# Kernel optimization log

Hardware: AMD Instinct MI355X
Metric: run time of the kernel (lower is better)

Reference implementation:

```python
import jax, jax.numpy as jnp
import numpy as np

N, C, T, V = 64, 64, 256, 25
REL, OUT = 8, 64
ALPHA = 1.0


def setup_inputs() -> dict:
    key = jax.random.key(0)
    ks = jax.random.split(key, 10)
    s = lambda k, shape: jax.random.normal(k, shape, dtype=jnp.float32) * 0.05
    return {
        "x": jax.random.normal(ks[0], (N, C, T, V), dtype=jnp.float32),
        "A": jax.random.normal(ks[1], (V, V), dtype=jnp.float32),
        "w1": s(ks[2], (REL, C)), "b1": s(ks[3], (REL,)),
        "w2": s(ks[4], (REL, C)), "b2": s(ks[5], (REL,)),
        "w3": s(ks[6], (OUT, C)), "b3": s(ks[7], (OUT,)),
        "w4": s(ks[8], (OUT, REL)), "b4": s(ks[9], (OUT,)),
    }


def reference(x, A, w1, b1, w2, b2, w3, b3, w4, b4):
    # 1x1 conv commutes with the temporal mean, so reduce T first (same math).
    xm = jnp.mean(x, axis=2)                                   # [N, C, V]
    x1 = jnp.einsum('ncv,rc->nrv', xm, w1) + b1[:, None]        # [N, R, V]
    x2 = jnp.einsum('ncv,rc->nrv', xm, w2) + b2[:, None]        # [N, R, V]
    x3 = jnp.einsum('nctv,oc->notv', x, w3) + b3[:, None, None] # [N, O, T, V]
    # dynamic topology: tanh of broadcast difference -> [N, R, V, V]
    adj = jnp.tanh(x1[:, :, :, None] - x2[:, :, None, :])
    # conv4 (1x1 over VxV) then scale + static adjacency
    d = jnp.einsum('nruv,or->nouv', adj, w4) + b4[:, None, None]
    d = d * ALPHA + A[None, None]                               # [N, O, V, V]
    # graph aggregation: out[n,o,t,v] = sum_u d[n,o,u,v] * x3[n,o,t,u]
    return jnp.einsum('nouv,notu->notv', d, x3)
```

## Files before the change

kernel.cpp:

```cpp
#include <hip/hip_runtime.h>

#define N_ 64
#define C_ 64
#define T_ 256
#define V_ 25
#define R_ 8
#define O_ 64
constexpr int TV = T_ * V_;
constexpr float INV_T = 1.0f / (float)T_;
constexpr int TC = 16;
constexpr int NPOS = TC * V_;
constexpr int NT = NPOS / 16;
constexpr int DP = 32;
constexpr int UPAD = 40;
constexpr int X3S = 16 * UPAD + 8;

typedef __attribute__((ext_vector_type(8))) short s8v;
typedef __attribute__((ext_vector_type(4))) short s4v;
typedef __attribute__((ext_vector_type(4))) float f4v;

__device__ __forceinline__ unsigned short f2bf(float f) {
    union { float f; unsigned u; } v; v.f = f;
    unsigned r = v.u + 0x7FFFu + ((v.u >> 16) & 1u);
    return (unsigned short)(r >> 16);
}

__global__ __launch_bounds__(256) void k_mean(const float* __restrict__ x,
                                              float* __restrict__ xm) {
    __shared__ float part[8 * V_];
    const int bid = blockIdx.x;
    const int tid = threadIdx.x;
    const float* xp = x + (size_t)bid * TV;
    if (tid < 200) {
        const int vid = tid % V_;
        const int seg = tid / V_;
        float s = 0.f;
        const float* p = xp + seg * 32 * V_ + vid;
        #pragma unroll
        for (int j = 0; j < 32; ++j) s += p[j * V_];
        part[tid] = s;
    }
    __syncthreads();
    if (tid < V_) {
        float s = 0.f;
        #pragma unroll
        for (int k = 0; k < 8; ++k) s += part[k * V_ + tid];
        xm[(size_t)bid * V_ + tid] = s * INV_T;
    }
}

__global__ __launch_bounds__(256) void k_dmat(const float* __restrict__ xm,
                                              const float* __restrict__ A,
                                              const float* __restrict__ w1,
                                              const float* __restrict__ b1,
                                              const float* __restrict__ w2,
                                              const float* __restrict__ b2,
                                              const float* __restrict__ w4,
                                              const float* __restrict__ b4,
                                              unsigned short* __restrict__ dT) {
    __shared__ float xms[C_][V_];
    __shared__ float x1s[R_][V_];
    __shared__ float x2s[R_][V_];
    const int n  = blockIdx.x;
    const int og = blockIdx.y * 8;
    const int tid = threadIdx.x;

    for (int i = tid; i < C_ * V_; i += 256)
        xms[i / V_][i % V_] = xm[(size_t)n * C_ * V_ + i];
    __syncthreads();

    for (int i = tid; i < 2 * R_ * V_; i += 256) {
        const int j = i % (R_ * V_);
        const int r = j / V_, v = j % V_;
        const bool first = (i < R_ * V_);
        const float* w = first ? w1 : w2;
        float acc = first ? b1[r] : b2[r];
        #pragma unroll
        for (int c = 0; c < C_; ++c) acc += w[r * C_ + c] * xms[c][v];
        if (first) x1s[r][v] = acc;
        else       x2s[r][v] = acc;
    }
    __syncthreads();

    unsigned short* dn = dT + (size_t)n * O_ * DP * DP;
    for (int p = tid; p < DP * DP; p += 256) {
        const int v = p >> 5, u = p & 31;
        if (u < V_ && v < V_) {
            float adjr[R_];
            #pragma unroll
            for (int r = 0; r < R_; ++r) adjr[r] = tanhf(x1s[r][u] - x2s[r][v]);
            const float a = A[u * V_ + v];
            #pragma unroll
            for (int oo = 0; oo < 8; ++oo) {
                const int o = og + oo;
                float acc = b4[o];
                #pragma unroll
                for (int r = 0; r < R_; ++r) acc = fmaf(w4[o * R_ + r], adjr[r], acc);
                dn[(size_t)o * DP * DP + p] = f2bf(acc + a);
            }
        } else {
            #pragma unroll
            for (int oo = 0; oo < 8; ++oo)
                dn[(size_t)(og + oo) * DP * DP + p] = 0;
        }
    }
}

__global__ __launch_bounds__(512) void k_F(const float* __restrict__ x,
                                           const float* __restrict__ w3,
                                           const float* __restrict__ b3,
                                           const unsigned short* __restrict__ dT,
                                           float* __restrict__ out) {
    __shared__ __align__(16) unsigned short x3b[16 * X3S];

    const int n    = blockIdx.y;
    const int tc   = blockIdx.x;
    const int tid  = threadIdx.x;
    const int lane = tid & 63;
    const int wave = tid >> 6;
    const int l16  = lane & 15;
    const int lg   = lane >> 4;

    if (tid < 256) {
        const int o_l = tid >> 4, t = tid & 15;
        *(s8v*)&x3b[o_l * X3S + t * UPAD + 24] = (s8v)0;
    }
    __syncthreads();

    const float* xbase = x + (size_t)n * C_ * TV + tc * NPOS;
    s8v bfr[4][2];
    #pragma unroll
    for (int i = 0; i < 4; ++i) {
        const int nt = wave + 8 * i;
        if (nt < NT) {
            const int pos = nt * 16 + l16;
            #pragma unroll
            for (int kh = 0; kh < 2; ++kh) {
                s8v f;
                #pragma unroll
                for (int j = 0; j < 8; ++j)
                    f[j] = (short)f2bf(xbase[(size_t)(kh * 32 + lg * 8 + j) * TV + pos]);
                bfr[i][kh] = f;
            }
        }
    }

    const unsigned short* dn = dT + (size_t)n * O_ * DP * DP;
    float* on = out + (size_t)n * O_ * TV + tc * NPOS;

    #pragma unroll 1
    for (int h = 0; h < 4; ++h) {
        s8v afr[2];
        #pragma unroll
        for (int kh = 0; kh < 2; ++kh) {
            const float* wp = w3 + (h * 16 + l16) * C_ + kh * 32 + lg * 8;
            s8v f;
            #pragma unroll
            for (int j = 0; j < 8; ++j) f[j] = (short)f2bf(wp[j]);
            afr[kh] = f;
        }
        const f4v b3h = *(const f4v*)(b3 + h * 16 + lg * 4);

        #pragma unroll
        for (int i = 0; i < 4; ++i) {
            const int nt = wave + 8 * i;
            if (nt < NT) {
                const int pos = nt * 16 + l16;
                const int t = pos / 25, u = pos - 25 * t;
                f4v acc = (f4v)0.f;
                acc = __builtin_amdgcn_mfma_f32_16x16x32_bf16(afr[0], bfr[i][0], acc, 0, 0, 0);
                acc = __builtin_amdgcn_mfma_f32_16x16x32_bf16(afr[1], bfr[i][1], acc, 0, 0, 0);
                #pragma unroll
                for (int r = 0; r < 4; ++r)
                    x3b[(lg * 4 + r) * X3S + t * UPAD + u] = f2bf(acc[r] + b3h[r]);
            }
        }
        __syncthreads();

        #pragma unroll
        for (int oo = 0; oo < 2; ++oo) {
            const int o_l = wave * 2 + oo;
            const int o_g = h * 16 + o_l;
            const unsigned short* dp = dn + (size_t)o_g * DP * DP;
            const s8v bv0 = *(const s8v*)(dp + l16 * DP + lg * 8);
            const s8v bv1 = *(const s8v*)(dp + (16 + l16) * DP + lg * 8);
            const s8v av  = *(const s8v*)&x3b[o_l * X3S + l16 * UPAD + lg * 8];
            f4v c0 = (f4v)0.f, c1 = (f4v)0.f;
            c0 = __builtin_amdgcn_mfma_f32_16x16x32_bf16(av, bv0, c0, 0, 0, 0);
            c1 = __builtin_amdgcn_mfma_f32_16x16x32_bf16(av, bv1, c1, 0, 0, 0);
            float* ob = on + (size_t)o_g * TV;
            #pragma unroll
            for (int r = 0; r < 4; ++r) {
                const int t = lg * 4 + r;
                ob[t * 25 + l16] = c0[r];
                if (l16 < 9) ob[t * 25 + 16 + l16] = c1[r];
            }
        }
        __syncthreads();
    }
}

extern "C" void kernel_launch(void* const* d_in, const int* in_sizes, int n_in,
                              void* d_out, int out_size, void* d_ws, size_t ws_size,
                              hipStream_t stream) {
    const float* x  = (const float*)d_in[0];
    const float* A  = (const float*)d_in[1];
    const float* w1 = (const float*)d_in[2];
    const float* b1 = (const float*)d_in[3];
    const float* w2 = (const float*)d_in[4];
    const float* b2 = (const float*)d_in[5];
    const float* w3 = (const float*)d_in[6];
    const float* b3 = (const float*)d_in[7];
    const float* w4 = (const float*)d_in[8];
    const float* b4 = (const float*)d_in[9];

    float* out = (float*)d_out;
    float* xm  = (float*)d_ws;
    unsigned short* dTm = (unsigned short*)(xm + (size_t)N_ * C_ * V_);

    k_mean<<<N_ * C_, 256, 0, stream>>>(x, xm);
    k_dmat<<<dim3(N_, 8), 256, 0, stream>>>(xm, A, w1, b1, w2, b2, w4, b4, dTm);
    k_F<<<dim3(T_ / TC, N_), 512, 0, stream>>>(x, w3, b3, dTm, out);
}
```

Baseline: 86.82 us.

## Fuse temporal mean with bf16 transpose of x staged in output buffer

Replaces the per-channel mean kernel with a tiled prep kernel that loads x once through shared memory. It accumulates the temporal mean with atomics and writes a bf16 K-contiguous transposed copy of x into the output buffer as scratch. k_F then reads that packed copy with vector loads instead of strided scalar fp32 loads plus per-element conversion. This adds a memset, atomics and an extra write/read pass through the output buffer. Correctness depends on each k_F block consuming its own scratch region before overwriting it.

```diff
diff --git a/kernel.cpp b/kernel.cpp
--- a/kernel.cpp
+++ b/kernel.cpp
@@ -14,10 +14,12 @@
 constexpr int DP = 32;
 constexpr int UPAD = 40;
 constexpr int X3S = 16 * UPAD + 8;
+constexpr int CH = 32;
+constexpr int LROW = 402;
 
 typedef __attribute__((ext_vector_type(8))) short s8v;
-typedef __attribute__((ext_vector_type(4))) short s4v;
 typedef __attribute__((ext_vector_type(4))) float f4v;
+typedef __attribute__((ext_vector_type(2))) float f2v;
 
 __device__ __forceinline__ unsigned short f2bf(float f) {
     union { float f; unsigned u; } v; v.f = f;
@@ -25,27 +27,58 @@
     return (unsigned short)(r >> 16);
 }
 
-__global__ __launch_bounds__(256) void k_mean(const float* __restrict__ x,
-                                              float* __restrict__ xm) {
-    __shared__ float part[8 * V_];
-    const int bid = blockIdx.x;
+__global__ __launch_bounds__(256) void k_prep(const float* __restrict__ x,
+                                              float* __restrict__ xm,
+                                              float* out) {
+    __shared__ float lx[CH * LROW];
+    const int n   = blockIdx.y;
+    const int tc  = blockIdx.x;
     const int tid = threadIdx.x;
-    const float* xp = x + (size_t)bid * TV;
-    if (tid < 200) {
-        const int vid = tid % V_;
-        const int seg = tid / V_;
-        float s = 0.f;
-        const float* p = xp + seg * 32 * V_ + vid;
-        #pragma unroll
-        for (int j = 0; j < 32; ++j) s += p[j * V_];
-        part[tid] = s;
-    }
-    __syncthreads();
-    if (tid < V_) {
-        float s = 0.f;
-        #pragma unroll
-        for (int k = 0; k < 8; ++k) s += part[k * V_ + tid];
-        xm[(size_t)bid * V_ + tid] = s * INV_T;
+    const float* xb = x + (size_t)n * C_ * TV + tc * NPOS;
+    char* xTb = (char*)out + (size_t)n * O_ * TV * 4 + (size_t)tc * 1600;
+
+    #pragma unroll 1
+    for (int kh = 0; kh < 2; ++kh) {
+        #pragma unroll 1
+        for (int i = 0; i < 13; ++i) {
+            const int s = i * 256 + tid;
+            if (s < CH * 100) {
+                const int c = s / 100, p4 = s - c * 100;
+                const f4v v = *(const f4v*)(xb + (size_t)(kh * CH + c) * TV + p4 * 4);
+                float* p = &lx[c * LROW + p4 * 4];
+                *(f2v*)p = f2v{v[0], v[1]};
+                *(f2v*)(p + 2) = f2v{v[2], v[3]};
+            }
+        }
+        __syncthreads();
+
+        #pragma unroll 1
+        for (int i = 0; i < 4; ++i) {
+            const int p = i * 256 + tid;
+            if (p < CH * V_) {
+                const int c = p / V_, v = p - c * V_;
+                float s = 0.f;
+                #pragma unroll
+                for (int t = 0; t < TC; ++t) s += lx[c * LROW + t * V_ + v];
+                atomicAdd(&xm[(size_t)n * C_ * V_ + (kh * CH + c) * V_ + v], s * INV_T);
+            }
+        }
+
+        #pragma unroll 1
+        for (int i = 0; i < 7; ++i) {
+            const int it = i * 256 + tid;
+            if (it < 1600) {
+                const int pos = it >> 2, ch = it & 3;
+                s8v pk;
+                #pragma unroll
+                for (int j = 0; j < 8; ++j)
+                    pk[j] = (short)f2bf(lx[(ch * 8 + j) * LROW + pos]);
+                const int L = pos * 128 + kh * 64 + ch * 16;
+                const int row = L / 1600, off = L - row * 1600;
+                *(s8v*)(xTb + (size_t)row * (TV * 4) + off) = pk;
+            }
+        }
+        __syncthreads();
     }
 }
 
@@ -106,11 +139,10 @@
     }
 }
 
-__global__ __launch_bounds__(512) void k_F(const float* __restrict__ x,
-                                           const float* __restrict__ w3,
+__global__ __launch_bounds__(512) void k_F(const float* __restrict__ w3,
                                            const float* __restrict__ b3,
                                            const unsigned short* __restrict__ dT,
-                                           float* __restrict__ out) {
+                                           float* io) {
     __shared__ __align__(16) unsigned short x3b[16 * X3S];
 
     const int n    = blockIdx.y;
@@ -127,7 +159,7 @@
     }
     __syncthreads();
 
-    const float* xbase = x + (size_t)n * C_ * TV + tc * NPOS;
+    const char* xTb = (const char*)io + (size_t)n * O_ * TV * 4 + (size_t)tc * 1600;
     s8v bfr[4][2];
     #pragma unroll
     for (int i = 0; i < 4; ++i) {
@@ -136,17 +168,15 @@
             const int pos = nt * 16 + l16;
             #pragma unroll
             for (int kh = 0; kh < 2; ++kh) {
-                s8v f;
-                #pragma unroll
-                for (int j = 0; j < 8; ++j)
-                    f[j] = (short)f2bf(xbase[(size_t)(kh * 32 + lg * 8 + j) * TV + pos]);
-                bfr[i][kh] = f;
+                const int L = pos * 128 + kh * 64 + lg * 16;
+                const int row = L / 1600, off = L - row * 1600;
+                bfr[i][kh] = *(const s8v*)(xTb + (size_t)row * (TV * 4) + off);
             }
         }
     }
 
     const unsigned short* dn = dT + (size_t)n * O_ * DP * DP;
-    float* on = out + (size_t)n * O_ * TV + tc * NPOS;
+    float* on = io + (size_t)n * O_ * TV + tc * NPOS;
 
     #pragma unroll 1
     for (int h = 0; h < 4; ++h) {
@@ -218,7 +248,8 @@
     float* xm  = (float*)d_ws;
     unsigned short* dTm = (unsigned short*)(xm + (size_t)N_ * C_ * V_);
 
-    k_mean<<<N_ * C_, 256, 0, stream>>>(x, xm);
+    hipMemsetAsync(xm, 0, (size_t)N_ * C_ * V_ * sizeof(float), stream);
+    k_prep<<<dim3(T_ / TC, N_), 256, 0, stream>>>(x, xm, out);
     k_dmat<<<dim3(N_, 8), 256, 0, stream>>>(xm, A, w1, b1, w2, b2, w4, b4, dTm);
-    k_F<<<dim3(T_ / TC, N_), 512, 0, stream>>>(x, w3, b3, dTm, out);
-}
+    k_F<<<dim3(T_ / TC, N_), 512, 0, stream>>>(w3, b3, dTm, out);
+}
```

Measured after the change: 105.8 us. 1.22x slower.
